# Kernel tuning notes

Hardware: AMD Instinct MI355X
Metric: run time of the kernel (lower is better)

Reference implementation:

```python
import jax, jax.numpy as jnp
import numpy as np

KH, KW = 7, 7      # t2t kernel_size
ST = 3             # stride
PD = 3             # padding
K = KH * KW        # 49 taps per patch


def _patch_indices(H, W):
    """Linear indices into the padded (Hp,Wp) image for every (patch l, tap k)."""
    Hp, Wp = H + 2 * PD, W + 2 * PD
    oh = (H + 2 * PD - KH) // ST + 1
    ow = (W + 2 * PD - KW) // ST + 1
    ki, kj = np.meshgrid(np.arange(KH), np.arange(KW), indexing='ij')
    rows = (np.arange(oh) * ST)[:, None, None, None] + ki[None, None]   # (oh,1,kh,kw)
    cols = (np.arange(ow) * ST)[None, :, None, None] + kj[None, None]   # (1,ow,kh,kw)
    idx = (rows * Wp + cols).reshape(oh * ow, K)                        # (L, 49)
    return jnp.asarray(idx), Hp, Wp, oh * ow


def setup_inputs() -> dict:
    key = jax.random.key(0)
    k1, k2, k3 = jax.random.split(key, 3)
    b, n, d, hd = 2, 5760, 512, 1960
    return {
        'x': jax.random.normal(k1, (b, n, d), dtype=jnp.float32),
        'W1': jax.random.normal(k2, (d, hd), dtype=jnp.float32) * 0.02,
        'b1': jnp.zeros((hd,), dtype=jnp.float32),
        'W2': jax.random.normal(k3, (hd, d), dtype=jnp.float32) * 0.02,
        'b2': jnp.zeros((d,), dtype=jnp.float32),
        'out_h': 60,
        'out_w': 108,
    }


def reference(x, W1, b1, W2, b2, out_h, out_w):
    H, W = int(out_h), int(out_w)
    idx, Hp, Wp, L = _patch_indices(H, W)          # idx: (L, 49)
    idxf = idx.reshape(-1)                         # (L*49,)

    b, n, _ = x.shape
    h = x @ W1 + b1                                # (b, n, 1960)
    hd = h.shape[-1]
    C = hd // K                                    # 40 fold channels
    Bp = (b * n) // L                              # fold batch (= b * t)

    # fold input layout: (Bp, C, K, L) -> scatter-add into padded image
    patches = h.reshape(Bp, L, C, K)
    vals = jnp.transpose(patches, (0, 2, 1, 3)).reshape(Bp * C, L * K)
    img = jnp.zeros((Bp * C, Hp * Wp), x.dtype).at[:, idxf].add(vals)

    # overlap-count normalizer (fold of ones), same for every batch/channel
    count = jnp.zeros((Hp * Wp,), x.dtype).at[idxf].add(jnp.ones_like(idxf, x.dtype))

    # crop padding (as F.fold does), normalize, re-pad with zeros (as F.unfold does)
    img = img.reshape(Bp, C, Hp, Wp)[:, :, PD:PD + H, PD:PD + W]
    cnt = count.reshape(Hp, Wp)[PD:PD + H, PD:PD + W]
    img = img / cnt
    flat = jnp.pad(img, ((0, 0), (0, 0), (PD, PD), (PD, PD))).reshape(Bp * C, Hp * Wp)

    # unfold: gather the same taps back, restore (b, n, hd) token layout
    g = flat[:, idxf].reshape(Bp, C, L, K)
    g = jnp.transpose(g, (0, 2, 1, 3)).reshape(b, n, hd)

    return jax.nn.gelu(g, approximate=False) @ W2 + b2
```

## Files before the change

kernel.cpp:

```cpp
#include <hip/hip_runtime.h>

typedef _Float16 f16;
typedef __attribute__((ext_vector_type(8))) _Float16 half8;
typedef __attribute__((ext_vector_type(4))) _Float16 half4;
typedef __attribute__((ext_vector_type(4))) float f32x4;

#define LDS_AS __attribute__((address_space(3)))
#define GLB_AS __attribute__((address_space(1)))

__device__ __forceinline__ void load16_lds(const f16* g, f16* l) {
    __builtin_amdgcn_global_load_lds((GLB_AS void*)(g), (LDS_AS void*)(l), 16, 0, 0);
}

#define WAIT8_BARRIER()  asm volatile("s_waitcnt vmcnt(8)\n\ts_barrier" ::: "memory")
#define WAIT4_BARRIER()  asm volatile("s_waitcnt vmcnt(4)\n\ts_barrier" ::: "memory")
#define WAIT0_BARRIER()  asm volatile("s_waitcnt vmcnt(0)\n\ts_barrier" ::: "memory")
#define ENDBAR()         asm volatile("s_waitcnt lgkmcnt(0)\n\ts_barrier" ::: "memory")

__global__ __launch_bounds__(256, 3) void gemm1(
    const f16* __restrict__ A, const f16* __restrict__ Bt,
    const float* __restrict__ bias, f16* __restrict__ C)
{
    const int id  = blockIdx.x;
    const int xcd = id & 7;
    const int r   = id >> 3;
    const int mt  = r & 15;
    const int nt  = xcd + 8 * (r >> 4);
    if (nt >= 90) return;
    const int m0 = mt * 128, n0 = nt * 128;
    const int K = 512, ldc = 11520;

    __shared__ f16 As[2][128 * 32];
    __shared__ f16 Bs[2][128 * 32];
    const int tid  = threadIdx.x;
    const int wave = tid >> 6;
    const int lane = tid & 63;

    const int s0 = tid, s1 = tid + 256;
    const f16* gA0 = A  + (m0 + (s0 >> 2)) * K + (s0 & 3) * 8;
    const f16* gA1 = A  + (m0 + (s1 >> 2)) * K + (s1 & 3) * 8;
    const f16* gB0 = Bt + (n0 + (s0 >> 2)) * K + (s0 & 3) * 8;
    const f16* gB1 = Bt + (n0 + (s1 >> 2)) * K + (s1 & 3) * 8;

    const int wm = (wave >> 1) * 64;
    const int wn = (wave & 1) * 64;
    const int lr = lane & 15;
    const int k8 = (lane >> 4) * 8;

    f32x4 acc[4][4];
#pragma unroll
    for (int i = 0; i < 4; ++i)
#pragma unroll
        for (int j = 0; j < 4; ++j) acc[i][j] = f32x4{0.f, 0.f, 0.f, 0.f};

#define G1_ISSUE(st, k0) do { \
    load16_lds(gA0 + (k0), &As[st][wave * 512]); \
    load16_lds(gA1 + (k0), &As[st][2048 + wave * 512]); \
    load16_lds(gB0 + (k0), &Bs[st][wave * 512]); \
    load16_lds(gB1 + (k0), &Bs[st][2048 + wave * 512]); \
} while (0)

    G1_ISSUE(0, 0);
    const int NS = 16;
    for (int s = 0; s < NS; ++s) {
        const int cur = s & 1;
        if (s + 1 < NS) {
            G1_ISSUE(cur ^ 1, (s + 1) * 32);
            WAIT4_BARRIER();
        } else {
            WAIT0_BARRIER();
        }
        half8 af[4], bf[4];
#pragma unroll
        for (int i = 0; i < 4; ++i)
            af[i] = *(const half8*)&As[cur][(wm + i * 16 + lr) * 32 + k8];
#pragma unroll
        for (int j = 0; j < 4; ++j)
            bf[j] = *(const half8*)&Bs[cur][(wn + j * 16 + lr) * 32 + k8];
#pragma unroll
        for (int i = 0; i < 4; ++i)
#pragma unroll
            for (int j = 0; j < 4; ++j)
                acc[i][j] = __builtin_amdgcn_mfma_f32_16x16x32_f16(
                    af[i], bf[j], acc[i][j], 0, 0, 0);
        ENDBAR();
    }

#pragma unroll
    for (int i = 0; i < 4; ++i) {
#pragma unroll
        for (int rr = 0; rr < 4; ++rr) {
            const int row = m0 + wm + i * 16 + (lane >> 4) * 4 + rr;
            const float bvr = (row < 1960) ? bias[row] : 0.f;
#pragma unroll
            for (int j = 0; j < 4; ++j) {
                const int col = n0 + wn + j * 16 + lr;
                C[row * ldc + col] = (f16)(acc[i][j][rr] + bvr);
            }
        }
    }
}

__global__ __launch_bounds__(256, 2) void gemm2(
    const f16* __restrict__ A, const f16* __restrict__ Bt,
    const float* __restrict__ bias, float* __restrict__ Cout)
{
    const int id  = blockIdx.x;
    const int xcd = id & 7;
    const int j2  = id >> 3;
    const int nt  = j2 & 3;
    const int mt  = (j2 >> 2) * 8 + xcd;
    if (mt >= 90) return;
    const int m0 = mt * 128, n0 = nt * 128;

    __shared__ f16 smem[24576];
    const int tid  = threadIdx.x;
    const int wave = tid >> 6;
    const int lane = tid & 63;

    const int s1 = tid + 256;
    const f16* gA0 = A  + (m0 + (tid >> 2)) * 2048 + (tid & 3) * 8;
    const f16* gA1 = A  + (m0 + (s1 >> 2)) * 2048 + (s1 & 3) * 8;
    const f16* gB0 = Bt + (n0 + (tid >> 2)) * 2048 + (tid & 3) * 8;
    const f16* gB1 = Bt + (n0 + (s1 >> 2)) * 2048 + (s1 & 3) * 8;

    const int wm = (wave >> 1) * 64;
    const int wn = (wave & 1) * 64;
    const int lr = lane & 15;
    const int k8 = (lane >> 4) * 8;

    f32x4 acc[4][4];
#pragma unroll
    for (int i = 0; i < 4; ++i)
#pragma unroll
        for (int j = 0; j < 4; ++j) acc[i][j] = f32x4{0.f, 0.f, 0.f, 0.f};

#define G2_ISSUE(st, k0) do { \
    f16* sb_ = &smem[(st) * 8192]; \
    load16_lds(gA0 + (k0), sb_ + wave * 512); \
    load16_lds(gA1 + (k0), sb_ + 2048 + wave * 512); \
    load16_lds(gB0 + (k0), sb_ + 4096 + wave * 512); \
    load16_lds(gB1 + (k0), sb_ + 6144 + wave * 512); \
} while (0)

    G2_ISSUE(0, 0);
    G2_ISSUE(1, 32);
    const int NS = 64;
    int cur = 0;
    for (int s = 0; s < NS; ++s) {
        if (s + 2 < NS) {
            int pre = cur + 2; if (pre >= 3) pre -= 3;
            G2_ISSUE(pre, (s + 2) * 32);
        }
        const int rem = NS - 1 - s;
        if (rem >= 2)      WAIT8_BARRIER();
        else if (rem == 1) WAIT4_BARRIER();
        else               WAIT0_BARRIER();
        const f16* sa = &smem[cur * 8192];
        half8 af[4], bf[4];
#pragma unroll
        for (int i = 0; i < 4; ++i)
            af[i] = *(const half8*)&sa[(wm + i * 16 + lr) * 32 + k8];
#pragma unroll
        for (int j = 0; j < 4; ++j)
            bf[j] = *(const half8*)&sa[4096 + (wn + j * 16 + lr) * 32 + k8];
#pragma unroll
        for (int i = 0; i < 4; ++i)
#pragma unroll
            for (int j = 0; j < 4; ++j)
                acc[i][j] = __builtin_amdgcn_mfma_f32_16x16x32_f16(
                    af[i], bf[j], acc[i][j], 0, 0, 0);
        ENDBAR();
        ++cur; if (cur >= 3) cur = 0;
    }

#pragma unroll
    for (int j = 0; j < 4; ++j) {
        const int col = n0 + wn + j * 16 + lr;
        const float bv = bias[col];
#pragma unroll
        for (int i = 0; i < 4; ++i) {
            const int rbase = m0 + wm + i * 16 + (lane >> 4) * 4;
#pragma unroll
            for (int rr = 0; rr < 4; ++rr)
                Cout[(rbase + rr) * 512 + col] = acc[i][j][rr] + bv;
        }
    }
}

__global__ void fold_gelu(const f16* __restrict__ h_t, f16* __restrict__ imgG)
{
    const int r  = blockIdx.x;
    const int bc = blockIdx.y;
    const int bp  = bc / 40;
    const int cch = bc % 40;
    const int c = threadIdx.x;
    if (c >= 114) return;
    float outv = 0.f;
    if (r >= 3 && r < 63 && c >= 3 && c < 111) {
        const int qr = r / 3, rm = r % 3;
        const int qc = c / 3, cm = c % 3;
        int kis[3], ohs[3], nr = 0;
        int kjs[3], ows[3], nc = 0;
#pragma unroll
        for (int t = 0; t < 3; ++t) {
            const int ki = rm + 3 * t, oh = qr - t;
            if (ki < 7 && oh >= 0 && oh < 20) { kis[nr] = ki; ohs[nr] = oh; ++nr; }
            const int kj = cm + 3 * t, ow = qc - t;
            if (kj < 7 && ow >= 0 && ow < 36) { kjs[nc] = kj; ows[nc] = ow; ++nc; }
        }
        float sum = 0.f;
        for (int a = 0; a < nr; ++a)
            for (int b = 0; b < nc; ++b) {
                const int n = cch * 49 + kis[a] * 7 + kjs[b];
                const int token = bp * 720 + ohs[a] * 36 + ows[b];
                sum += (float)h_t[n * 11520 + token];
            }
        const float xv = sum / (float)(nr * nc);
        outv = 0.5f * xv * (1.f + erff(xv * 0.70710678118654752f));
    }
    imgG[(bc * 66 + r) * 114 + c] = (f16)outv;
}

__global__ __launch_bounds__(256) void unfold_lds(
    const f16* __restrict__ imgG, f16* __restrict__ g16)
{
    __shared__ f16 ch[7524];
    const int bc = blockIdx.x;
    const int bp = bc / 40, cch = bc % 40;
    const float* src = (const float*)(imgG + bc * 7524);
    float* dst = (float*)ch;
    for (int i = threadIdx.x; i < 3762; i += 256) dst[i] = src[i];
    __syncthreads();
    const int tokbase = bp * 720;
    const int colbase = cch * 49;
    for (int flat = threadIdx.x; flat < 35280; flat += 256) {
        const int l = flat / 49, k = flat - l * 49;
        const int oh = l / 36, ow = l - oh * 36;
        const int ki = k / 7,  kj = k - ki * 7;
        g16[(tokbase + l) * 2048 + colbase + k] =
            ch[(oh * 3 + ki) * 114 + ow * 3 + kj];
    }
    if (cch >= 36) {
        const int cb = 1960 + (cch - 36) * 22;
        for (int flat = threadIdx.x; flat < 720 * 22; flat += 256) {
            const int l = flat / 22, k = flat - l * 22;
            g16[(tokbase + l) * 2048 + cb + k] = (f16)0.f;
        }
    }
}

__global__ __launch_bounds__(256) void prep(
    const float* __restrict__ x, f16* __restrict__ xh,
    const float* __restrict__ W1, f16* __restrict__ W1t,
    const float* __restrict__ W2, f16* __restrict__ W2t)
{
    __shared__ float tile[32][33];
    const int b = blockIdx.x, t = threadIdx.x;
    if (b < 5760) {
        const int i = b * 256 + t;
        const float4 v = ((const float4*)x)[i];
        half4 o;
        o[0] = (f16)v.x; o[1] = (f16)v.y; o[2] = (f16)v.z; o[3] = (f16)v.w;
        ((half4*)xh)[i] = o;
        return;
    }
    const float* src; f16* dst; int R, C, Rp, Cp, bx, by;
    if (b < 6784) {
        const int local = b - 5760;
        bx = local & 15; by = local >> 4;
        src = W1; dst = W1t; R = 512; C = 1960; Rp = 512; Cp = 2048;
    } else {
        const int local = b - 6784;
        bx = local & 63; by = local >> 6;
        src = W2; dst = W2t; R = 1960; C = 512; Rp = 2048; Cp = 512;
    }
    const int r0 = bx * 32, c0 = by * 32;
    const int tx = t & 31, ty = t >> 5;
#pragma unroll
    for (int i = 0; i < 32; i += 8) {
        const int r = r0 + ty + i, c = c0 + tx;
        tile[ty + i][tx] = (r < R && c < C) ? src[r * C + c] : 0.f;
    }
    __syncthreads();
#pragma unroll
    for (int i = 0; i < 32; i += 8) {
        const int c = c0 + ty + i, r = r0 + tx;
        if (c < Cp && r < Rp) dst[c * Rp + r] = (f16)tile[tx][ty + i];
    }
}

extern "C" void kernel_launch(void* const* d_in, const int* in_sizes, int n_in,
                              void* d_out, int out_size, void* d_ws, size_t ws_size,
                              hipStream_t stream)
{
    const float* x  = (const float*)d_in[0];
    const float* W1 = (const float*)d_in[1];
    const float* b1 = (const float*)d_in[2];
    const float* W2 = (const float*)d_in[3];
    const float* b2 = (const float*)d_in[4];

    char* ws = (char*)d_ws;
    f16* xh   = (f16*)(ws);
    f16* W1t  = (f16*)(ws + 11796480);
    f16* W2t  = (f16*)(ws + 11796480 + 2097152);
    f16* hbuf = (f16*)(ws + 11796480 + 2 * 2097152);
    f16* imgG = (f16*)(ws + 11796480 + 2 * 2097152 + 47185920);

    prep<<<dim3(7808), dim3(256), 0, stream>>>(x, xh, W1, W1t, W2, W2t);
    gemm1<<<dim3(1536), dim3(256), 0, stream>>>(W1t, xh, b1, hbuf);
    fold_gelu<<<dim3(66, 640), dim3(128), 0, stream>>>(hbuf, imgG);
    unfold_lds<<<dim3(640), dim3(256), 0, stream>>>(imgG, hbuf);
    gemm2<<<dim3(384), dim3(256), 0, stream>>>(hbuf, W2t, b2, (float*)d_out);
}
```

Measured before the change: 226.9 us.

## Fuse fold+gelu into unfold kernel and triple-buffer gemm1 loads

Merges the fold/GELU kernel into the unfold kernel so each block computes its channel image straight into LDS, removing the imgG round trip through global memory and one launch. Because the fused kernel cannot write in place over its input, it now writes to a separate g16 buffer. Separately, gemm1 moves to a 3-stage LDS ring with two loads in flight, to hide more global latency at the cost of extra LDS (48KB), which may reduce occupancy under launch_bounds(256,3). The fused kernel has only 640 blocks doing the gather and erf work, so it has less parallelism than the old 42k-block fold.

Result: slower. 253.9 us (+11.9%).

```diff
diff --git a/kernel.cpp b/kernel.cpp
--- a/kernel.cpp
+++ b/kernel.cpp
@@ -30,16 +30,15 @@
     const int m0 = mt * 128, n0 = nt * 128;
     const int K = 512, ldc = 11520;
 
-    __shared__ f16 As[2][128 * 32];
-    __shared__ f16 Bs[2][128 * 32];
+    __shared__ f16 smem[24576];
     const int tid  = threadIdx.x;
     const int wave = tid >> 6;
     const int lane = tid & 63;
 
-    const int s0 = tid, s1 = tid + 256;
-    const f16* gA0 = A  + (m0 + (s0 >> 2)) * K + (s0 & 3) * 8;
+    const int s1 = tid + 256;
+    const f16* gA0 = A  + (m0 + (tid >> 2)) * K + (tid & 3) * 8;
     const f16* gA1 = A  + (m0 + (s1 >> 2)) * K + (s1 & 3) * 8;
-    const f16* gB0 = Bt + (n0 + (s0 >> 2)) * K + (s0 & 3) * 8;
+    const f16* gB0 = Bt + (n0 + (tid >> 2)) * K + (tid & 3) * 8;
     const f16* gB1 = Bt + (n0 + (s1 >> 2)) * K + (s1 & 3) * 8;
 
     const int wm = (wave >> 1) * 64;
@@ -54,29 +53,34 @@
         for (int j = 0; j < 4; ++j) acc[i][j] = f32x4{0.f, 0.f, 0.f, 0.f};
 
 #define G1_ISSUE(st, k0) do { \
-    load16_lds(gA0 + (k0), &As[st][wave * 512]); \
-    load16_lds(gA1 + (k0), &As[st][2048 + wave * 512]); \
-    load16_lds(gB0 + (k0), &Bs[st][wave * 512]); \
-    load16_lds(gB1 + (k0), &Bs[st][2048 + wave * 512]); \
+    f16* sb_ = &smem[(st) * 8192]; \
+    load16_lds(gA0 + (k0), sb_ + wave * 512); \
+    load16_lds(gA1 + (k0), sb_ + 2048 + wave * 512); \
+    load16_lds(gB0 + (k0), sb_ + 4096 + wave * 512); \
+    load16_lds(gB1 + (k0), sb_ + 6144 + wave * 512); \
 } while (0)
 
     G1_ISSUE(0, 0);
+    G1_ISSUE(1, 32);
     const int NS = 16;
+    int cur = 0;
     for (int s = 0; s < NS; ++s) {
-        const int cur = s & 1;
-        if (s + 1 < NS) {
-            G1_ISSUE(cur ^ 1, (s + 1) * 32);
-            WAIT4_BARRIER();
-        } else {
-            WAIT0_BARRIER();
-        }
+        if (s + 2 < NS) {
+            int pre = cur + 2; if (pre >= 3) pre -= 3;
+            G1_ISSUE(pre, (s + 2) * 32);
+        }
+        const int rem = NS - 1 - s;
+        if (rem >= 2)      WAIT8_BARRIER();
+        else if (rem == 1) WAIT4_BARRIER();
+        else               WAIT0_BARRIER();
+        const f16* sa = &smem[cur * 8192];
         half8 af[4], bf[4];
 #pragma unroll
         for (int i = 0; i < 4; ++i)
-            af[i] = *(const half8*)&As[cur][(wm + i * 16 + lr) * 32 + k8];
+            af[i] = *(const half8*)&sa[(wm + i * 16 + lr) * 32 + k8];
 #pragma unroll
         for (int j = 0; j < 4; ++j)
-            bf[j] = *(const half8*)&Bs[cur][(wn + j * 16 + lr) * 32 + k8];
+            bf[j] = *(const half8*)&sa[4096 + (wn + j * 16 + lr) * 32 + k8];
 #pragma unroll
         for (int i = 0; i < 4; ++i)
 #pragma unroll
@@ -84,6 +88,7 @@
                 acc[i][j] = __builtin_amdgcn_mfma_f32_16x16x32_f16(
                     af[i], bf[j], acc[i][j], 0, 0, 0);
         ENDBAR();
+        ++cur; if (cur >= 3) cur = 0;
     }
 
 #pragma unroll
@@ -188,50 +193,42 @@
     }
 }
 
-__global__ void fold_gelu(const f16* __restrict__ h_t, f16* __restrict__ imgG)
-{
-    const int r  = blockIdx.x;
-    const int bc = blockIdx.y;
-    const int bp  = bc / 40;
-    const int cch = bc % 40;
-    const int c = threadIdx.x;
-    if (c >= 114) return;
-    float outv = 0.f;
-    if (r >= 3 && r < 63 && c >= 3 && c < 111) {
-        const int qr = r / 3, rm = r % 3;
-        const int qc = c / 3, cm = c % 3;
-        int kis[3], ohs[3], nr = 0;
-        int kjs[3], ows[3], nc = 0;
-#pragma unroll
-        for (int t = 0; t < 3; ++t) {
-            const int ki = rm + 3 * t, oh = qr - t;
-            if (ki < 7 && oh >= 0 && oh < 20) { kis[nr] = ki; ohs[nr] = oh; ++nr; }
-            const int kj = cm + 3 * t, ow = qc - t;
-            if (kj < 7 && ow >= 0 && ow < 36) { kjs[nc] = kj; ows[nc] = ow; ++nc; }
-        }
-        float sum = 0.f;
-        for (int a = 0; a < nr; ++a)
-            for (int b = 0; b < nc; ++b) {
-                const int n = cch * 49 + kis[a] * 7 + kjs[b];
-                const int token = bp * 720 + ohs[a] * 36 + ows[b];
-                sum += (float)h_t[n * 11520 + token];
-            }
-        const float xv = sum / (float)(nr * nc);
-        outv = 0.5f * xv * (1.f + erff(xv * 0.70710678118654752f));
-    }
-    imgG[(bc * 66 + r) * 114 + c] = (f16)outv;
-}
-
-__global__ __launch_bounds__(256) void unfold_lds(
-    const f16* __restrict__ imgG, f16* __restrict__ g16)
+__global__ __launch_bounds__(256) void fold_unfold(
+    const f16* __restrict__ h_t, f16* __restrict__ g16)
 {
     __shared__ f16 ch[7524];
     const int bc = blockIdx.x;
     const int bp = bc / 40, cch = bc % 40;
-    const float* src = (const float*)(imgG + bc * 7524);
-    float* dst = (float*)ch;
-    for (int i = threadIdx.x; i < 3762; i += 256) dst[i] = src[i];
+
+    for (int flat = threadIdx.x; flat < 7524; flat += 256) {
+        const int r = flat / 114, c = flat - r * 114;
+        float outv = 0.f;
+        if (r >= 3 && r < 63 && c >= 3 && c < 111) {
+            const int qr = r / 3, rm = r % 3;
+            const int qc = c / 3, cm = c % 3;
+            int kis[3], ohs[3], nr = 0;
+            int kjs[3], ows[3], nc = 0;
+#pragma unroll
+            for (int t = 0; t < 3; ++t) {
+                const int ki = rm + 3 * t, oh = qr - t;
+                if (ki < 7 && oh >= 0 && oh < 20) { kis[nr] = ki; ohs[nr] = oh; ++nr; }
+                const int kj = cm + 3 * t, ow = qc - t;
+                if (kj < 7 && ow >= 0 && ow < 36) { kjs[nc] = kj; ows[nc] = ow; ++nc; }
+            }
+            float sum = 0.f;
+            for (int a = 0; a < nr; ++a)
+                for (int b = 0; b < nc; ++b) {
+                    const int n = cch * 49 + kis[a] * 7 + kjs[b];
+                    const int token = bp * 720 + ohs[a] * 36 + ows[b];
+                    sum += (float)h_t[n * 11520 + token];
+                }
+            const float xv = sum / (float)(nr * nc);
+            outv = 0.5f * xv * (1.f + erff(xv * 0.70710678118654752f));
+        }
+        ch[flat] = (f16)outv;
+    }
     __syncthreads();
+
     const int tokbase = bp * 720;
     const int colbase = cch * 49;
     for (int flat = threadIdx.x; flat < 35280; flat += 256) {
@@ -304,12 +301,11 @@
     f16* xh   = (f16*)(ws);
     f16* W1t  = (f16*)(ws + 11796480);
     f16* W2t  = (f16*)(ws + 11796480 + 2097152);
-    f16* hbuf = (f16*)(ws + 11796480 + 2 * 2097152);
-    f16* imgG = (f16*)(ws + 11796480 + 2 * 2097152 + 47185920);
+    f16* h_t  = (f16*)(ws + 11796480 + 2 * 2097152);
+    f16* g16  = (f16*)(ws + 11796480 + 2 * 2097152 + 47185920);
 
     prep<<<dim3(7808), dim3(256), 0, stream>>>(x, xh, W1, W1t, W2, W2t);
-    gemm1<<<dim3(1536), dim3(256), 0, stream>>>(W1t, xh, b1, hbuf);
-    fold_gelu<<<dim3(66, 640), dim3(128), 0, stream>>>(hbuf, imgG);
-    unfold_lds<<<dim3(640), dim3(256), 0, stream>>>(imgG, hbuf);
-    gemm2<<<dim3(384), dim3(256), 0, stream>>>(hbuf, W2t, b2, (float*)d_out);
-}
+    gemm1<<<dim3(1536), dim3(256), 0, stream>>>(W1t, xh, b1, h_t);
+    fold_unfold<<<dim3(640), dim3(256), 0, stream>>>(h_t, g16);
+    gemm2<<<dim3(384), dim3(256), 0, stream>>>(g16, W2t, b2, (float*)d_out);
+}
```
